# Optimization experiments

Measured on AMD Instinct MI355X. Metric: run time of the kernel, lower is better.

The kernel has to match this reference:

```python
import jax, jax.numpy as jnp
import numpy as np

N_QUBITS = 4
Q_DEPTH = 2


def _apply_rx(st, theta, wire):
    # st: (N, 2,2,2,2) complex; RX(theta) on `wire` (axis wire+1)
    theta = jnp.broadcast_to(jnp.asarray(theta, st.real.dtype), (st.shape[0],))
    half = theta * 0.5
    bshape = (-1,) + (1,) * (N_QUBITS - 1)
    c = jnp.cos(half).reshape(bshape)
    s = jnp.sin(half).reshape(bshape)
    a0 = jax.lax.index_in_dim(st, 0, axis=wire + 1, keepdims=False)
    a1 = jax.lax.index_in_dim(st, 1, axis=wire + 1, keepdims=False)
    new0 = c * a0 - 1j * s * a1
    new1 = c * a1 - 1j * s * a0
    return jnp.stack([new0, new1], axis=wire + 1)


def _apply_cnot(st, ctrl, tgt):
    p0 = jax.lax.index_in_dim(st, 0, axis=ctrl + 1, keepdims=True)
    p1 = jax.lax.index_in_dim(st, 1, axis=ctrl + 1, keepdims=True)
    p1 = jnp.flip(p1, axis=tgt + 1)  # flip target bit where control = 1
    return jnp.concatenate([p0, p1], axis=ctrl + 1)


def quantum_layer(q_input, q_weights):
    # q_input: (N, n_qubits) angles; q_weights: (q_depth, n_qubits)
    N = q_input.shape[0]
    st = jnp.zeros((N,) + (2,) * N_QUBITS, jnp.complex64)
    st = st.at[(slice(None),) + (0,) * N_QUBITS].set(1.0)  # |0...0>
    # AngleEmbedding with rotation='X'
    for w in range(N_QUBITS):
        st = _apply_rx(st, q_input[:, w], w)
    # BasicEntanglerLayers: RX per wire then CNOT ring per layer
    for l in range(Q_DEPTH):
        for w in range(N_QUBITS):
            st = _apply_rx(st, q_weights[l, w], w)
        for w in range(N_QUBITS):
            st = _apply_cnot(st, w, (w + 1) % N_QUBITS)
    p = jnp.real(st) ** 2 + jnp.imag(st) ** 2  # probabilities (N,2,2,2,2)
    outs = []
    for w in range(N_QUBITS):
        axes = tuple(a for a in range(1, N_QUBITS + 1) if a != w + 1)
        m = p.sum(axis=axes)  # (N,2) marginal on wire w
        outs.append(m[:, 0] - m[:, 1])  # <PauliZ_w>
    return jnp.stack(outs, axis=1).astype(jnp.float32)


def setup_inputs() -> dict:
    key = jax.random.key(0)
    ks = jax.random.split(key, 6)
    B, T, D_IN, EMB, OUT = 256, 512, 32, 128, 10
    return {
        "inputs": jax.random.normal(ks[0], (B, T, D_IN), jnp.float32),
        "w_in": jax.random.normal(ks[1], (EMB, D_IN), jnp.float32) * 0.05,
        "b_in": jnp.zeros((EMB,), jnp.float32),
        "w_cip": jax.random.normal(ks[2], (4, EMB), jnp.float32) * 0.05,
        "q_weights": jax.random.uniform(ks[3], (Q_DEPTH, N_QUBITS), jnp.float32, 0.0, 2.0 * np.pi),
        "w_coe": jax.random.normal(ks[4], (EMB, 4), jnp.float32) * 0.05,
        "w_head": jax.random.normal(ks[5], (OUT, EMB), jnp.float32) * 0.05,
    }


def reference(inputs, w_in, b_in, w_cip, q_weights, w_coe, w_head):
    B, T, _ = inputs.shape
    x = inputs @ w_in.T + b_in                 # (B,T,EMB) input_proj
    xr = x.reshape(B * T, -1)
    q_in = xr @ w_cip.T                        # (B*T, n_qubits)
    q_out = quantum_layer(q_in, q_weights)     # (B*T, n_qubits) PauliZ expvals
    expanded = q_out @ w_coe.T                 # (B*T, EMB)
    preds = expanded.reshape(B, T, -1) @ w_head.T  # (B,T,OUT)
    return preds
```

## Files before the change

### kernel.cpp

```cpp
#include <hip/hip_runtime.h>
#include <math.h>

#define BB    256
#define TT    512
#define D_IN  32
#define EMB   128
#define NOUT  10
#define NQ    4
#define QD    2
#define NTOT  (BB * TT)

__device__ __forceinline__ void apply_rx(float re[16], float im[16],
                                         const int mask, const float c, const float s) {
#pragma unroll
    for (int i = 0; i < 16; ++i) {
        if (i & mask) continue;
        const int j = i | mask;
        const float r0 = re[i], i0 = im[i], r1 = re[j], i1 = im[j];
        re[i] = c * r0 + s * i1;
        im[i] = c * i0 - s * r1;
        re[j] = c * r1 + s * i0;
        im[j] = c * i1 - s * r0;
    }
}

__global__ __launch_bounds__(256) void qnn_fused_kernel(
    const float* __restrict__ inputs,
    const float* __restrict__ w_in,
    const float* __restrict__ b_in,
    const float* __restrict__ w_cip,
    const float* __restrict__ q_weights,
    const float* __restrict__ w_coe,
    const float* __restrict__ w_head,
    float* __restrict__ out)
{
    __shared__ float sM[NQ * D_IN];
    __shared__ float sC[NQ];
    __shared__ float sW2[NOUT * NQ];
    __shared__ float sCW[QD * NQ];
    __shared__ float sSW[QD * NQ];

    const int tid = threadIdx.x;
    if (tid < 128) {
        const int j = tid >> 5, d = tid & 31;
        float acc = 0.f;
#pragma unroll 8
        for (int e = 0; e < EMB; ++e)
            acc += w_cip[j * EMB + e] * w_in[e * D_IN + d];
        sM[tid] = acc;
    } else if (tid < 168) {
        const int k = tid - 128;
        const int o = k >> 2, j = k & 3;
        float acc = 0.f;
#pragma unroll 8
        for (int e = 0; e < EMB; ++e)
            acc += w_head[o * EMB + e] * w_coe[e * NQ + j];
        sW2[k] = acc;
    } else if (tid < 172) {
        const int j = tid - 168;
        float acc = 0.f;
        for (int e = 0; e < EMB; ++e)
            acc += w_cip[j * EMB + e] * b_in[e];
        sC[j] = acc;
    } else if (tid < 180) {
        const int k = tid - 172;
        const float h = q_weights[k] * 0.5f;
        sCW[k] = cosf(h);
        sSW[k] = sinf(h);
    }
    __syncthreads();

    const int bt = blockIdx.x * 256 + tid;
    if (bt >= NTOT) return;

    float xin[D_IN];
    const float4* ip = reinterpret_cast<const float4*>(inputs + (size_t)bt * D_IN);
#pragma unroll
    for (int k = 0; k < D_IN / 4; ++k) {
        const float4 v = ip[k];
        xin[k * 4 + 0] = v.x; xin[k * 4 + 1] = v.y;
        xin[k * 4 + 2] = v.z; xin[k * 4 + 3] = v.w;
    }

    float q[NQ];
#pragma unroll
    for (int j = 0; j < NQ; ++j) {
        float acc = sC[j];
#pragma unroll
        for (int d = 0; d < D_IN; ++d) acc += xin[d] * sM[j * D_IN + d];
        q[j] = acc;
    }

    float re[16], im[16];
#pragma unroll
    for (int i = 0; i < 16; ++i) { re[i] = 0.f; im[i] = 0.f; }
    re[0] = 1.f;

#pragma unroll
    for (int w = 0; w < NQ; ++w) {
        float s, c;
        sincosf(q[w] * 0.5f, &s, &c);
        apply_rx(re, im, 8 >> w, c, s);
    }

#pragma unroll
    for (int l = 0; l < QD; ++l) {
#pragma unroll
        for (int w = 0; w < NQ; ++w)
            apply_rx(re, im, 8 >> w, sCW[l * NQ + w], sSW[l * NQ + w]);
#pragma unroll
        for (int w = 0; w < NQ; ++w) {
            const int cm = 8 >> w;
            const int tm = 8 >> ((w + 1) & 3);
#pragma unroll
            for (int i = 0; i < 16; ++i) {
                if ((i & cm) && !(i & tm)) {
                    const int i2 = i | tm;
                    const float tr = re[i]; re[i] = re[i2]; re[i2] = tr;
                    const float ti = im[i]; im[i] = im[i2]; im[i2] = ti;
                }
            }
        }
    }

    float p[16];
#pragma unroll
    for (int i = 0; i < 16; ++i) p[i] = re[i] * re[i] + im[i] * im[i];

    float z[NQ];
#pragma unroll
    for (int w = 0; w < NQ; ++w) {
        const int m = 8 >> w;
        float acc = 0.f;
#pragma unroll
        for (int i = 0; i < 16; ++i) acc += (i & m) ? -p[i] : p[i];
        z[w] = acc;
    }

    float* op = out + (size_t)bt * NOUT;
#pragma unroll
    for (int o = 0; o < NOUT; ++o) {
        float acc = 0.f;
#pragma unroll
        for (int j = 0; j < NQ; ++j) acc += z[j] * sW2[o * NQ + j];
        op[o] = acc;
    }
}

extern "C" void kernel_launch(void* const* d_in, const int* in_sizes, int n_in,
                              void* d_out, int out_size, void* d_ws, size_t ws_size,
                              hipStream_t stream) {
    const float* inputs    = (const float*)d_in[0];
    const float* w_in      = (const float*)d_in[1];
    const float* b_in      = (const float*)d_in[2];
    const float* w_cip     = (const float*)d_in[3];
    const float* q_weights = (const float*)d_in[4];
    const float* w_coe     = (const float*)d_in[5];
    const float* w_head    = (const float*)d_in[6];
    float* out = (float*)d_out;

    const int threads = 256;
    const int blocks = (NTOT + threads - 1) / threads;
    qnn_fused_kernel<<<blocks, threads, 0, stream>>>(
        inputs, w_in, b_in, w_cip, q_weights, w_coe, w_head, out);
}
```

Before: 15.31 us.

## Precompute fused weights in a prep kernel and load them in the main kernel

Moves the per-block weight folding (w_cip·w_in, w_head·w_coe, bias, rotation cos/sin) into a single-block prep kernel that writes to workspace. The main kernel copies 188 floats into shared memory and overlaps that with the input load before a barrier. It also switches to the fast __sincosf intrinsic, writes the output as float2 stores, and drops the bounds check. The cost is a second kernel launch plus a serial dependency between the two kernels, and the fast sincos carries a small accuracy risk.

```diff
diff --git a/kernel.cpp b/kernel.cpp
--- a/kernel.cpp
+++ b/kernel.cpp
@@ -9,6 +9,8 @@
 #define NQ    4
 #define QD    2
 #define NTOT  (BB * TT)
+
+#define WS_FLOATS 188
 
 __device__ __forceinline__ void apply_rx(float re[16], float im[16],
                                          const int mask, const float c, const float s) {
@@ -24,22 +26,15 @@
     }
 }
 
-__global__ __launch_bounds__(256) void qnn_fused_kernel(
-    const float* __restrict__ inputs,
+__global__ __launch_bounds__(256) void qnn_prep_kernel(
     const float* __restrict__ w_in,
     const float* __restrict__ b_in,
     const float* __restrict__ w_cip,
     const float* __restrict__ q_weights,
     const float* __restrict__ w_coe,
     const float* __restrict__ w_head,
-    float* __restrict__ out)
+    float* __restrict__ fused)
 {
-    __shared__ float sM[NQ * D_IN];
-    __shared__ float sC[NQ];
-    __shared__ float sW2[NOUT * NQ];
-    __shared__ float sCW[QD * NQ];
-    __shared__ float sSW[QD * NQ];
-
     const int tid = threadIdx.x;
     if (tid < 128) {
         const int j = tid >> 5, d = tid & 31;
@@ -47,7 +42,7 @@
 #pragma unroll 8
         for (int e = 0; e < EMB; ++e)
             acc += w_cip[j * EMB + e] * w_in[e * D_IN + d];
-        sM[tid] = acc;
+        fused[tid] = acc;
     } else if (tid < 168) {
         const int k = tid - 128;
         const int o = k >> 2, j = k & 3;
@@ -55,23 +50,37 @@
 #pragma unroll 8
         for (int e = 0; e < EMB; ++e)
             acc += w_head[o * EMB + e] * w_coe[e * NQ + j];
-        sW2[k] = acc;
+        fused[tid] = acc;
     } else if (tid < 172) {
         const int j = tid - 168;
         float acc = 0.f;
         for (int e = 0; e < EMB; ++e)
             acc += w_cip[j * EMB + e] * b_in[e];
-        sC[j] = acc;
+        fused[tid] = acc;
     } else if (tid < 180) {
         const int k = tid - 172;
         const float h = q_weights[k] * 0.5f;
-        sCW[k] = cosf(h);
-        sSW[k] = sinf(h);
+        fused[tid] = cosf(h);
+        fused[tid + 8] = sinf(h);
     }
-    __syncthreads();
+}
+
+__global__ __launch_bounds__(256) void qnn_main_kernel(
+    const float* __restrict__ inputs,
+    const float* __restrict__ fused,
+    float* __restrict__ out)
+{
+    __shared__ float sF[WS_FLOATS];
+    const int tid = threadIdx.x;
+    if (tid < WS_FLOATS) sF[tid] = fused[tid];
+
+    const float* sM  = sF;
+    const float* sW2 = sF + 128;
+    const float* sC  = sF + 168;
+    const float* sCW = sF + 172;
+    const float* sSW = sF + 180;
 
     const int bt = blockIdx.x * 256 + tid;
-    if (bt >= NTOT) return;
 
     float xin[D_IN];
     const float4* ip = reinterpret_cast<const float4*>(inputs + (size_t)bt * D_IN);
@@ -81,6 +90,8 @@
         xin[k * 4 + 0] = v.x; xin[k * 4 + 1] = v.y;
         xin[k * 4 + 2] = v.z; xin[k * 4 + 3] = v.w;
     }
+
+    __syncthreads();
 
     float q[NQ];
 #pragma unroll
@@ -99,7 +110,7 @@
 #pragma unroll
     for (int w = 0; w < NQ; ++w) {
         float s, c;
-        sincosf(q[w] * 0.5f, &s, &c);
+        __sincosf(q[w] * 0.5f, &s, &c);
         apply_rx(re, im, 8 >> w, c, s);
     }
 
@@ -137,14 +148,18 @@
         z[w] = acc;
     }
 
-    float* op = out + (size_t)bt * NOUT;
+    float ov[NOUT];
 #pragma unroll
     for (int o = 0; o < NOUT; ++o) {
         float acc = 0.f;
 #pragma unroll
         for (int j = 0; j < NQ; ++j) acc += z[j] * sW2[o * NQ + j];
-        op[o] = acc;
+        ov[o] = acc;
     }
+    float2* op = reinterpret_cast<float2*>(out + (size_t)bt * NOUT);
+#pragma unroll
+    for (int o = 0; o < NOUT / 2; ++o)
+        op[o] = make_float2(ov[2 * o], ov[2 * o + 1]);
 }
 
 extern "C" void kernel_launch(void* const* d_in, const int* in_sizes, int n_in,
@@ -157,10 +172,9 @@
     const float* q_weights = (const float*)d_in[4];
     const float* w_coe     = (const float*)d_in[5];
     const float* w_head    = (const float*)d_in[6];
-    float* out = (float*)d_out;
+    float* out   = (float*)d_out;
+    float* fused = (float*)d_ws;
 
-    const int threads = 256;
-    const int blocks = (NTOT + threads - 1) / threads;
-    qnn_fused_kernel<<<blocks, threads, 0, stream>>>(
-        inputs, w_in, b_in, w_cip, q_weights, w_coe, w_head, out);
+    qnn_prep_kernel<<<1, 256, 0, stream>>>(w_in, b_in, w_cip, q_weights, w_coe, w_head, fused);
+    qnn_main_kernel<<<NTOT / 256, 256, 0, stream>>>(inputs, fused, out);
 }
```

Result: slower. 15.97 us (+4.3%).
